# Performance work log

Hardware: AMD Instinct MI355X
Metric: run time of the kernel (lower is better)

Reference implementation:

```python
import jax, jax.numpy as jnp
import numpy as np

BSZ, L, D_Q, S_Q = 2, 2048, 512, 4
EPS = 1e-6


def quat_mul(a, b):
    ar, ai, aj, ak = a[..., 0], a[..., 1], a[..., 2], a[..., 3]
    br, bi, bj, bk = b[..., 0], b[..., 1], b[..., 2], b[..., 3]
    return jnp.stack((
        ar * br - ai * bi - aj * bj - ak * bk,
        ar * bi + ai * br + aj * bk - ak * bj,
        ar * bj - ai * bk + aj * br + ak * bi,
        ar * bk + ai * bj - aj * bi + ak * br,
    ), axis=-1)


def quat_inv(q):
    r, i, j, k = q[..., 0], q[..., 1], q[..., 2], q[..., 3]
    s = 1.0 / (r * r + i * i + j * j + k * k + EPS)
    return jnp.stack((r * s, -i * s, -j * s, -k * s), axis=-1)


def setup_inputs() -> dict:
    key = jax.random.key(0)
    ks = jax.random.split(key, 8)
    u = jax.random.normal(ks[0], (BSZ, L, D_Q, 4), dtype=jnp.float32)
    dt = jax.random.uniform(ks[1], (BSZ, L, D_Q), dtype=jnp.float32)
    B_in = jax.random.normal(ks[2], (BSZ, L, S_Q, 4), dtype=jnp.float32)
    C_in = jax.random.normal(ks[3], (BSZ, L, S_Q, 4), dtype=jnp.float32)
    # A_log init: log(arange(1, S_q+1)) repeated over D_q rows
    A_log = jnp.tile(jnp.log(jnp.arange(1, S_Q + 1, dtype=jnp.float32)), (D_Q, 1))
    A_i = jax.random.normal(ks[4], (D_Q, S_Q), dtype=jnp.float32) * 0.01
    A_j = jax.random.normal(ks[5], (D_Q, S_Q), dtype=jnp.float32) * 0.01
    A_k = jax.random.normal(ks[6], (D_Q, S_Q), dtype=jnp.float32) * 0.01
    return {"u": u, "dt": dt, "B_in": B_in, "C_in": C_in,
            "A_log": A_log, "A_i": A_i, "A_j": A_j, "A_k": A_k}


def reference(u, dt, B_in, C_in, A_log, A_i, A_j, A_k):
    # A quaternion: real part -exp(A_log), imaginary parts A_i/j/k  [D_q, S_q, 4]
    A_quat = jnp.stack([-jnp.exp(A_log), A_i, A_j, A_k], axis=-1)
    dt_b = dt[..., None, None]                      # [B, L, D_q, 1, 1]
    z = dt_b * A_quat                               # [B, L, D_q, S_q, 4]
    one = jnp.zeros_like(z).at[..., 0].set(1.0)     # quaternion identity
    num = one + 0.5 * z
    den = one - 0.5 * z
    den_inv = quat_inv(den)
    q = quat_mul(den_inv, num)                      # Cayley transition [B,L,D_q,S_q,4]
    dB = quat_mul(den_inv * dt_b, B_in[:, :, None])  # [B,L,D_q,S_q,4]
    Bu = quat_mul(dB, u[:, :, :, None])             # [B,L,D_q,S_q,4]

    def step(h, qb):
        qt, but = qb
        h = quat_mul(qt, h) + but
        return h, h

    h0 = jnp.zeros((u.shape[0], u.shape[2], A_quat.shape[1], 4), u.dtype)
    _, h_all = jax.lax.scan(step, h0, (jnp.swapaxes(q, 0, 1), jnp.swapaxes(Bu, 0, 1)))
    h_all = jnp.swapaxes(h_all, 0, 1)               # [B, L, D_q, S_q, 4]
    yh = quat_mul(C_in[:, :, None], h_all)
    return yh.sum(axis=3)                           # [B, L, D_q, 4]
```

## Files before the change

### kernel.cpp

```cpp
#include <hip/hip_runtime.h>

#define BSZ   2
#define LSEQ  2048
#define DQ    512
#define SQ    4
#define EPSQ  1e-6f

typedef float nfloat4 __attribute__((ext_vector_type(4)));
typedef float nfloat2 __attribute__((ext_vector_type(2)));

__device__ __forceinline__ nfloat2 mk2(float x, float y) { nfloat2 v; v.x = x; v.y = y; return v; }

struct PQuat { nfloat2 ri, jk; };

__device__ __forceinline__ PQuat pq_of(const float4 v) {
    PQuat p; p.ri = mk2(v.x, v.y); p.jk = mk2(v.z, v.w); return p;
}
__device__ __forceinline__ float4 f4_of(const PQuat p) {
    return make_float4(p.ri.x, p.ri.y, p.jk.x, p.jk.y);
}

__device__ __forceinline__ PQuat pqmul(const PQuat a, const PQuat b) {
    const float ar = a.ri.x, ai = a.ri.y, aj = a.jk.x, ak = a.jk.y;
    PQuat o;
    o.ri = ar*b.ri + ai*mk2(-b.ri.y,  b.ri.x)
         + aj*mk2(-b.jk.x,  b.jk.y) + ak*mk2(-b.jk.y, -b.jk.x);
    o.jk = ar*b.jk + ai*mk2(-b.jk.y,  b.jk.x)
         + aj*mk2( b.ri.x, -b.ri.y) + ak*mk2( b.ri.y,  b.ri.x);
    return o;
}

__device__ __forceinline__ PQuat pqmuladd(const PQuat a, const PQuat b, const PQuat c) {
    const float ar = a.ri.x, ai = a.ri.y, aj = a.jk.x, ak = a.jk.y;
    PQuat o;
    o.ri = c.ri + ar*b.ri + ai*mk2(-b.ri.y,  b.ri.x)
         + aj*mk2(-b.jk.x,  b.jk.y) + ak*mk2(-b.jk.y, -b.jk.x);
    o.jk = c.jk + ar*b.jk + ai*mk2(-b.jk.y,  b.jk.x)
         + aj*mk2( b.ri.x, -b.ri.y) + ak*mk2( b.ri.y,  b.ri.x);
    return o;
}

struct HA { float r, i; nfloat2 jk; float p2, n2r; };

__device__ __forceinline__ HA load_hA(const float* __restrict__ Alog,
                                      const float* __restrict__ Ai,
                                      const float* __restrict__ Aj,
                                      const float* __restrict__ Ak, int idx) {
    HA h;
    h.r  = -0.5f * __expf(Alog[idx]);
    h.i  =  0.5f * Ai[idx];
    h.jk = mk2(0.5f * Aj[idx], 0.5f * Ak[idx]);
    h.p2 = h.r*h.r + h.i*h.i + h.jk.x*h.jk.x + h.jk.y*h.jk.y;
    h.n2r = -2.0f * h.r;
    return h;
}

__device__ __forceinline__ void cayley_pk(const float a, const float aa, const HA& hA,
                                          const PQuat B, const PQuat U,
                                          PQuat& q, PQuat& Bu) {
    const float dd = __builtin_fmaf(aa, hA.p2, __builtin_fmaf(a, hA.n2r, 1.0f + EPSQ));
    const float sv = __builtin_amdgcn_rcpf(dd);
    const float nr = __builtin_fmaf(-aa, hA.p2, 1.0f);
    const float as = a * sv;
    const float s2a = as + as;
    q.ri = mk2(nr * sv, s2a * hA.i);
    q.jk = s2a * hA.jk;
    PQuat cd;
    cd.ri = mk2(__builtin_fmaf(-a, hA.r, 1.0f), a * hA.i);
    cd.jk = a * hA.jk;
    const PQuat cb = pqmul(cd, B);
    PQuat dB; dB.ri = as * cb.ri; dB.jk = as * cb.jk;
    Bu = pqmul(dB, U);
}

struct Quat { float r, i, j, k; };
__device__ __forceinline__ Quat qmul(const Quat a, const Quat b) {
    Quat o;
    o.r = a.r*b.r - a.i*b.i - a.j*b.j - a.k*b.k;
    o.i = a.r*b.i + a.i*b.r + a.j*b.k - a.k*b.j;
    o.j = a.r*b.j - a.i*b.k + a.j*b.r + a.k*b.i;
    o.k = a.r*b.k + a.i*b.j - a.j*b.i + a.k*b.r;
    return o;
}
__device__ __forceinline__ Quat qmuladd(const Quat a, const Quat b, const Quat c) {
    Quat o;
    o.r = c.r + a.r*b.r - a.i*b.i - a.j*b.j - a.k*b.k;
    o.i = c.i + a.r*b.i + a.i*b.r + a.j*b.k - a.k*b.j;
    o.j = c.j + a.r*b.j - a.i*b.k + a.j*b.r + a.k*b.i;
    o.k = c.k + a.r*b.k + a.i*b.j - a.j*b.i + a.k*b.r;
    return o;
}
__device__ __forceinline__ Quat q_of(const float4 v) { return Quat{v.x, v.y, v.z, v.w}; }
__device__ __forceinline__ float4 f4s_of(const Quat q) { return make_float4(q.r, q.i, q.j, q.k); }

typedef unsigned int u32_t;
__device__ __forceinline__ void gl_lds16(const void* g, void* l) {
    __builtin_amdgcn_global_load_lds(
        (const __attribute__((address_space(1))) u32_t*)g,
        (__attribute__((address_space(3))) u32_t*)l, 16, 0, 0);
}
__device__ __forceinline__ void gl_lds4(const void* g, void* l) {
    __builtin_amdgcn_global_load_lds(
        (const __attribute__((address_space(1))) u32_t*)g,
        (__attribute__((address_space(3))) u32_t*)l, 4, 0, 0);
}

template<int NCH>
__global__ __launch_bounds__(256, 6) void qssm_pass1(
    const float* __restrict__ u, const float* __restrict__ dt,
    const float* __restrict__ Bin,
    const float* __restrict__ Alog, const float* __restrict__ Ai,
    const float* __restrict__ Aj,   const float* __restrict__ Ak,
    float4* __restrict__ WQ, float4* __restrict__ WB)
{
    constexpr int CH = LSEQ / NCH;
    __shared__ float4 uL[CH][128];
    __shared__ float  dtL[CH][128];
    __shared__ float4 BL[CH][SQ];

    const int t    = threadIdx.x;
    const int lane = t & 63;
    const int wid  = t >> 6;
    const int dblk = blockIdx.x;
    const int c    = blockIdx.y;
    const int b    = blockIdx.z;
    const int t0   = c * CH;
    const int base = b*LSEQ + t0;

    const float4* ug  = (const float4*)u + (size_t)base*DQ + dblk*128;
    const float*  dtg = dt + (size_t)base*DQ + dblk*128;
    const float*  Bg  = Bin + (size_t)base*SQ*4;
#pragma unroll
    for (int jj = 0; jj < CH/4; ++jj) {
        const int j = wid*(CH/4) + jj;
#pragma unroll
        for (int k = 0; k < 2; ++k) {
            gl_lds16(ug  + (size_t)j*DQ + k*64 + lane, &uL[j][k*64]);
            gl_lds4 (dtg + (size_t)j*DQ + k*64 + lane, &dtL[j][k*64]);
        }
    }
    if (wid == 0) {
#pragma unroll
        for (int k = 0; k < 2; ++k)
            gl_lds4(Bg + k*64 + lane, ((float*)BL) + k*64);
    }

    const int dl = t & 127;
    const int sh = t >> 7;
    const int s0 = sh * 2;
    const int d  = dblk*128 + dl;

    HA hA0 = load_hA(Alog, Ai, Aj, Ak, d*SQ + s0);
    HA hA1 = load_hA(Alog, Ai, Aj, Ak, d*SQ + s0 + 1);

    __syncthreads();

    PQuat Q[2], Bc[2];
    {
        const float a  = dtL[0][dl];
        const float aa = a * a;
        const PQuat U  = pq_of(uL[0][dl]);
        PQuat q, Bu;
        cayley_pk(a, aa, hA0, pq_of(BL[0][s0]),     U, q, Bu);
        Q[0] = q; Bc[0] = Bu;
        cayley_pk(a, aa, hA1, pq_of(BL[0][s0 + 1]), U, q, Bu);
        Q[1] = q; Bc[1] = Bu;
    }
#pragma unroll
    for (int j = 1; j < CH; ++j) {
        const float a  = dtL[j][dl];
        const float aa = a * a;
        const PQuat U  = pq_of(uL[j][dl]);
        PQuat q, Bu;
        cayley_pk(a, aa, hA0, pq_of(BL[j][s0]),     U, q, Bu);
        Bc[0] = pqmuladd(q, Bc[0], Bu);
        Q[0]  = pqmul(q, Q[0]);
        cayley_pk(a, aa, hA1, pq_of(BL[j][s0 + 1]), U, q, Bu);
        Bc[1] = pqmuladd(q, Bc[1], Bu);
        Q[1]  = pqmul(q, Q[1]);
    }
#pragma unroll
    for (int ss = 0; ss < 2; ++ss) {
        const size_t idx = ((size_t)(b*SQ + s0 + ss)*NCH + c)*DQ + d;
        WQ[idx] = f4_of(Q[ss]);
        WB[idx] = f4_of(Bc[ss]);
    }
}

template<int NCH>
__global__ __launch_bounds__(512) void qssm_pass2(
    const float4* __restrict__ WQ, float4* __restrict__ WB)
{
    constexpr int GS = 8;
    constexpr int NG = NCH / GS;
    __shared__ float4 QL[NG][16];
    __shared__ float4 BL2[NG][16];
    __shared__ float4 HS[NG][16];

    const int t  = threadIdx.x;
    const int i  = t & 15;
    const int g  = t >> 4;
    const int bs = blockIdx.x >> 5;
    const int d  = (blockIdx.x & 31) * 16 + i;
    const size_t chbase = (size_t)bs * NCH * DQ + d;

    size_t idx = chbase + (size_t)(g * GS) * DQ;
    Quat Qa = q_of(WQ[idx]);
    Quat Ba = q_of(WB[idx]);
#pragma unroll
    for (int j = 1; j < GS; ++j) {
        idx += DQ;
        const Quat Qc = q_of(WQ[idx]);
        const Quat Bc = q_of(WB[idx]);
        Ba = qmuladd(Qc, Ba, Bc);
        Qa = qmul(Qc, Qa);
    }
    QL[g][i]  = f4s_of(Qa);
    BL2[g][i] = f4s_of(Ba);
    __syncthreads();

    if (t < 16) {
        Quat h{0.f, 0.f, 0.f, 0.f};
#pragma unroll
        for (int gg = 0; gg < NG; ++gg) {
            HS[gg][t] = f4s_of(h);
            h = qmuladd(q_of(QL[gg][t]), h, q_of(BL2[gg][t]));
        }
    }
    __syncthreads();

    Quat h = q_of(HS[g][i]);
    idx = chbase + (size_t)(g * GS) * DQ;
#pragma unroll
    for (int j = 0; j < GS; ++j) {
        const Quat Qc = q_of(WQ[idx]);
        const Quat Bc = q_of(WB[idx]);
        WB[idx] = f4s_of(h);
        h = qmuladd(Qc, h, Bc);
        idx += DQ;
    }
}

template<int NCH>
__global__ __launch_bounds__(256, 6) void qssm_pass3(
    const float* __restrict__ u, const float* __restrict__ dt,
    const float* __restrict__ Bin, const float* __restrict__ Cin,
    const float* __restrict__ Alog, const float* __restrict__ Ai,
    const float* __restrict__ Aj,   const float* __restrict__ Ak,
    const float4* __restrict__ WB, float* __restrict__ out)
{
    constexpr int CH = LSEQ / NCH;
    __shared__ float4 uL[CH][128];
    __shared__ float  dtL[CH][128];
    __shared__ float4 BL[CH][SQ];
    __shared__ float4 CL[CH][SQ];

    const int t    = threadIdx.x;
    const int lane = t & 63;
    const int wid  = t >> 6;
    const int dblk = blockIdx.x;
    const int c    = blockIdx.y;
    const int b    = blockIdx.z;
    const int t0   = c * CH;
    const int base = b*LSEQ + t0;

    const float4* ug  = (const float4*)u + (size_t)base*DQ + dblk*128;
    const float*  dtg = dt + (size_t)base*DQ + dblk*128;
    const float*  Bg  = Bin + (size_t)base*SQ*4;
    const float*  Cg  = Cin + (size_t)base*SQ*4;
#pragma unroll
    for (int jj = 0; jj < CH/4; ++jj) {
        const int j = wid*(CH/4) + jj;
#pragma unroll
        for (int k = 0; k < 2; ++k) {
            gl_lds16(ug  + (size_t)j*DQ + k*64 + lane, &uL[j][k*64]);
            gl_lds4 (dtg + (size_t)j*DQ + k*64 + lane, &dtL[j][k*64]);
        }
    }
    if (wid == 0) {
#pragma unroll
        for (int k = 0; k < 2; ++k)
            gl_lds4(Bg + k*64 + lane, ((float*)BL) + k*64);
    } else if (wid == 1) {
#pragma unroll
        for (int k = 0; k < 2; ++k)
            gl_lds4(Cg + k*64 + lane, ((float*)CL) + k*64);
    }

    const int dl = lane & 31;
    const int sh = lane >> 5;
    const int s0 = sh * 2;
    const int dloc = wid*32 + dl;
    const int d    = dblk*128 + dloc;

    HA hA0 = load_hA(Alog, Ai, Aj, Ak, d*SQ + s0);
    HA hA1 = load_hA(Alog, Ai, Aj, Ak, d*SQ + s0 + 1);
    PQuat h0 = pq_of(WB[((size_t)(b*SQ + s0    )*NCH + c)*DQ + d]);
    PQuat h1 = pq_of(WB[((size_t)(b*SQ + s0 + 1)*NCH + c)*DQ + d]);

    nfloat4* outp = (nfloat4*)out + (size_t)base*DQ + d;

    __syncthreads();

#pragma unroll
    for (int j = 0; j < CH; ++j) {
        const float a  = dtL[j][dloc];
        const float aa = a * a;
        const PQuat U  = pq_of(uL[j][dloc]);
        PQuat y; y.ri = mk2(0.f, 0.f); y.jk = mk2(0.f, 0.f);
        PQuat q, Bu;
        cayley_pk(a, aa, hA0, pq_of(BL[j][s0]),     U, q, Bu);
        h0 = pqmuladd(q, h0, Bu);
        y  = pqmuladd(pq_of(CL[j][s0]),     h0, y);
        cayley_pk(a, aa, hA1, pq_of(BL[j][s0 + 1]), U, q, Bu);
        h1 = pqmuladd(q, h1, Bu);
        y  = pqmuladd(pq_of(CL[j][s0 + 1]), h1, y);
        float yr = y.ri.x + __shfl_xor(y.ri.x, 32);
        float yi = y.ri.y + __shfl_xor(y.ri.y, 32);
        float yj = y.jk.x + __shfl_xor(y.jk.x, 32);
        float yk = y.jk.y + __shfl_xor(y.jk.y, 32);
        if (sh == 0) {
            const nfloat4 yv = {yr, yi, yj, yk};
            __builtin_nontemporal_store(yv, outp);
        }
        outp += DQ;
    }
}

template<int NCH>
static void launch_all(const float* u, const float* dt, const float* Bin,
                       const float* Cin, const float* Alog, const float* Ai,
                       const float* Aj, const float* Ak,
                       float* out, void* d_ws, hipStream_t stream) {
    const size_t elems = (size_t)BSZ * SQ * NCH * DQ;
    float4* WQ = (float4*)d_ws;
    float4* WB = WQ + elems;
    dim3 g1(DQ / 128, NCH, BSZ);
    qssm_pass1<NCH><<<g1, 256, 0, stream>>>(u, dt, Bin, Alog, Ai, Aj, Ak, WQ, WB);
    qssm_pass2<NCH><<<(BSZ*SQ*DQ)/16, 16*(NCH/8), 0, stream>>>(WQ, WB);
    dim3 g3(DQ / 128, NCH, BSZ);
    qssm_pass3<NCH><<<g3, 256, 0, stream>>>(u, dt, Bin, Cin, Alog, Ai, Aj, Ak, WB, out);
}

extern "C" void kernel_launch(void* const* d_in, const int* in_sizes, int n_in,
                              void* d_out, int out_size, void* d_ws, size_t ws_size,
                              hipStream_t stream) {
    const float* u    = (const float*)d_in[0];
    const float* dt   = (const float*)d_in[1];
    const float* Bin  = (const float*)d_in[2];
    const float* Cin  = (const float*)d_in[3];
    const float* Alog = (const float*)d_in[4];
    const float* Ai   = (const float*)d_in[5];
    const float* Aj   = (const float*)d_in[6];
    const float* Ak   = (const float*)d_in[7];
    float* out = (float*)d_out;

    auto ws_need = [](int nch) -> size_t {
        return 2ull * BSZ * SQ * (size_t)nch * DQ * sizeof(float4);
    };
    if (ws_size >= ws_need(256)) {
        launch_all<256>(u, dt, Bin, Cin, Alog, Ai, Aj, Ak, out, d_ws, stream);
    } else if (ws_size >= ws_need(128)) {
        launch_all<128>(u, dt, Bin, Cin, Alog, Ai, Aj, Ak, out, d_ws, stream);
    } else {
        launch_all<64>(u, dt, Bin, Cin, Alog, Ai, Aj, Ak, out, d_ws, stream);
    }
}
```

Baseline: 151.7 us.

## Fuse three-pass chunked scan into one cooperative kernel with grid syncs

```diff
diff --git a/kernel.cpp b/kernel.cpp
--- a/kernel.cpp
+++ b/kernel.cpp
@@ -1,4 +1,7 @@
 #include <hip/hip_runtime.h>
+#include <hip/hip_cooperative_groups.h>
+
+namespace cg = cooperative_groups;
 
 #define BSZ   2
 #define LSEQ  2048
@@ -105,6 +108,186 @@
         (__attribute__((address_space(3))) u32_t*)l, 4, 0, 0);
 }
 
+#define NCHF 256
+#define CHF  (LSEQ / NCHF)
+#define NTF  (BSZ * NCHF * (DQ/128))
+
+union SMemF {
+    struct { float4 uL[CHF][128]; float dtL[CHF][128];
+             float4 BL[CHF][SQ];   float4 CL[CHF][SQ]; } ac;
+    struct { float4 QL[32][16]; float4 BL2[32][16]; float4 HS[32][16]; } b;
+};
+
+__global__ __launch_bounds__(512, 4) void qssm_fused2(
+    const float* __restrict__ u, const float* __restrict__ dt,
+    const float* __restrict__ Bin, const float* __restrict__ Cin,
+    const float* __restrict__ Alog, const float* __restrict__ Ai,
+    const float* __restrict__ Aj,   const float* __restrict__ Ak,
+    float4* __restrict__ WQ, float4* __restrict__ WB, float* __restrict__ out)
+{
+    __shared__ SMemF sm;
+    cg::grid_group grid = cg::this_grid();
+    const int t    = threadIdx.x;
+    const int lane = t & 63;
+    const int wid  = t >> 6;
+
+    {
+        const int dl = t & 127;
+        const int sq = t >> 7;
+        for (int tid = blockIdx.x; tid < NTF; tid += (int)gridDim.x) {
+            const int dblk = tid & 3;
+            const int c    = (tid >> 2) & (NCHF - 1);
+            const int b    =  tid >> 10;
+            const int base = b*LSEQ + c*CHF;
+
+            __syncthreads();
+            const float4* ug  = (const float4*)u + (size_t)base*DQ + dblk*128;
+            const float*  dtg = dt + (size_t)base*DQ + dblk*128;
+            const float*  Bg  = Bin + (size_t)base*SQ*4;
+            {
+                const int j = wid;
+#pragma unroll
+                for (int k = 0; k < 2; ++k) {
+                    gl_lds16(ug  + (size_t)j*DQ + k*64 + lane, &sm.ac.uL[j][k*64]);
+                    gl_lds4 (dtg + (size_t)j*DQ + k*64 + lane, &sm.ac.dtL[j][k*64]);
+                }
+            }
+            if (wid == 0) {
+#pragma unroll
+                for (int k = 0; k < (CHF*SQ*4)/64; ++k)
+                    gl_lds4(Bg + k*64 + lane, ((float*)sm.ac.BL) + k*64);
+            }
+            const int d = dblk*128 + dl;
+            const HA hA = load_hA(Alog, Ai, Aj, Ak, d*SQ + sq);
+            __syncthreads();
+
+            PQuat Q, Bc;
+            {
+                const float a = sm.ac.dtL[0][dl];
+                cayley_pk(a, a*a, hA, pq_of(sm.ac.BL[0][sq]), pq_of(sm.ac.uL[0][dl]), Q, Bc);
+            }
+#pragma unroll
+            for (int j = 1; j < CHF; ++j) {
+                const float a = sm.ac.dtL[j][dl];
+                PQuat q, Bu;
+                cayley_pk(a, a*a, hA, pq_of(sm.ac.BL[j][sq]), pq_of(sm.ac.uL[j][dl]), q, Bu);
+                Bc = pqmuladd(q, Bc, Bu);
+                Q  = pqmul(q, Q);
+            }
+            const size_t idx = ((size_t)(b*SQ + sq)*NCHF + c)*DQ + d;
+            WQ[idx] = f4_of(Q);
+            WB[idx] = f4_of(Bc);
+        }
+    }
+    grid.sync();
+
+    if (blockIdx.x < 256) {
+        constexpr int GS = 8;
+        constexpr int NG = NCHF / GS;
+        const int i  = t & 15;
+        const int g  = t >> 4;
+        const int bs = blockIdx.x >> 5;
+        const int d  = (blockIdx.x & 31) * 16 + i;
+        const size_t chbase = (size_t)bs * NCHF * DQ + d;
+
+        size_t idx = chbase + (size_t)(g * GS) * DQ;
+        Quat Qa = q_of(WQ[idx]);
+        Quat Ba = q_of(WB[idx]);
+#pragma unroll
+        for (int j = 1; j < GS; ++j) {
+            idx += DQ;
+            const Quat Qc = q_of(WQ[idx]);
+            const Quat Bc = q_of(WB[idx]);
+            Ba = qmuladd(Qc, Ba, Bc);
+            Qa = qmul(Qc, Qa);
+        }
+        sm.b.QL[g][i]  = f4s_of(Qa);
+        sm.b.BL2[g][i] = f4s_of(Ba);
+        __syncthreads();
+
+        if (t < 16) {
+            Quat h{0.f, 0.f, 0.f, 0.f};
+#pragma unroll
+            for (int gg = 0; gg < NG; ++gg) {
+                sm.b.HS[gg][t] = f4s_of(h);
+                h = qmuladd(q_of(sm.b.QL[gg][t]), h, q_of(sm.b.BL2[gg][t]));
+            }
+        }
+        __syncthreads();
+
+        Quat h = q_of(sm.b.HS[g][i]);
+        idx = chbase + (size_t)(g * GS) * DQ;
+#pragma unroll
+        for (int j = 0; j < GS; ++j) {
+            const Quat Qc = q_of(WQ[idx]);
+            const Quat Bc = q_of(WB[idx]);
+            WB[idx] = f4s_of(h);
+            h = qmuladd(Qc, h, Bc);
+            idx += DQ;
+        }
+    }
+    grid.sync();
+
+    {
+        const int dl   = lane & 15;
+        const int sq   = lane >> 4;
+        const int dloc = wid*16 + dl;
+        for (int tid = blockIdx.x; tid < NTF; tid += (int)gridDim.x) {
+            const int dblk = tid & 3;
+            const int c    = (tid >> 2) & (NCHF - 1);
+            const int b    =  tid >> 10;
+            const int base = b*LSEQ + c*CHF;
+
+            __syncthreads();
+            const float4* ug  = (const float4*)u + (size_t)base*DQ + dblk*128;
+            const float*  dtg = dt + (size_t)base*DQ + dblk*128;
+            const float*  Bg  = Bin + (size_t)base*SQ*4;
+            const float*  Cg  = Cin + (size_t)base*SQ*4;
+            {
+                const int j = wid;
+#pragma unroll
+                for (int k = 0; k < 2; ++k) {
+                    gl_lds16(ug  + (size_t)j*DQ + k*64 + lane, &sm.ac.uL[j][k*64]);
+                    gl_lds4 (dtg + (size_t)j*DQ + k*64 + lane, &sm.ac.dtL[j][k*64]);
+                }
+            }
+            if (wid == 0) {
+#pragma unroll
+                for (int k = 0; k < (CHF*SQ*4)/64; ++k)
+                    gl_lds4(Bg + k*64 + lane, ((float*)sm.ac.BL) + k*64);
+            } else if (wid == 1) {
+#pragma unroll
+                for (int k = 0; k < (CHF*SQ*4)/64; ++k)
+                    gl_lds4(Cg + k*64 + lane, ((float*)sm.ac.CL) + k*64);
+            }
+            const int d = dblk*128 + dloc;
+            const HA hA = load_hA(Alog, Ai, Aj, Ak, d*SQ + sq);
+            PQuat h = pq_of(WB[((size_t)(b*SQ + sq)*NCHF + c)*DQ + d]);
+            nfloat4* outp = (nfloat4*)out + (size_t)base*DQ + d;
+            __syncthreads();
+
+#pragma unroll
+            for (int j = 0; j < CHF; ++j) {
+                const float a = sm.ac.dtL[j][dloc];
+                PQuat q, Bu;
+                cayley_pk(a, a*a, hA, pq_of(sm.ac.BL[j][sq]), pq_of(sm.ac.uL[j][dloc]), q, Bu);
+                h = pqmuladd(q, h, Bu);
+                const PQuat y = pqmul(pq_of(sm.ac.CL[j][sq]), h);
+                float yr = y.ri.x, yi = y.ri.y, yj = y.jk.x, yk = y.jk.y;
+                yr += __shfl_xor(yr, 16); yi += __shfl_xor(yi, 16);
+                yj += __shfl_xor(yj, 16); yk += __shfl_xor(yk, 16);
+                yr += __shfl_xor(yr, 32); yi += __shfl_xor(yi, 32);
+                yj += __shfl_xor(yj, 32); yk += __shfl_xor(yk, 32);
+                if (sq == 0) {
+                    const nfloat4 yv = {yr, yi, yj, yk};
+                    __builtin_nontemporal_store(yv, outp);
+                }
+                outp += DQ;
+            }
+        }
+    }
+}
+
 template<int NCH>
 __global__ __launch_bounds__(256, 6) void qssm_pass1(
     const float* __restrict__ u, const float* __restrict__ dt,
@@ -124,8 +307,7 @@
     const int dblk = blockIdx.x;
     const int c    = blockIdx.y;
     const int b    = blockIdx.z;
-    const int t0   = c * CH;
-    const int base = b*LSEQ + t0;
+    const int base = b*LSEQ + c*CH;
 
     const float4* ug  = (const float4*)u + (size_t)base*DQ + dblk*128;
     const float*  dtg = dt + (size_t)base*DQ + dblk*128;
@@ -261,8 +443,7 @@
     const int dblk = blockIdx.x;
     const int c    = blockIdx.y;
     const int b    = blockIdx.z;
-    const int t0   = c * CH;
-    const int base = b*LSEQ + t0;
+    const int base = b*LSEQ + c*CH;
 
     const float4* ug  = (const float4*)u + (size_t)base*DQ + dblk*128;
     const float*  dtg = dt + (size_t)base*DQ + dblk*128;
@@ -287,9 +468,9 @@
             gl_lds4(Cg + k*64 + lane, ((float*)CL) + k*64);
     }
 
-    const int dl = lane & 31;
-    const int sh = lane >> 5;
-    const int s0 = sh * 2;
+    const int dl   = lane & 31;
+    const int sh   = lane >> 5;
+    const int s0   = sh * 2;
     const int dloc = wid*32 + dl;
     const int d    = dblk*128 + dloc;
 
@@ -355,6 +536,20 @@
     const float* Ak   = (const float*)d_in[7];
     float* out = (float*)d_out;
 
+    const size_t elemsF = (size_t)BSZ * SQ * NCHF * DQ;
+    if (ws_size >= 2 * elemsF * sizeof(float4)) {
+        float4* WQ = (float4*)d_ws;
+        float4* WB = WQ + elemsF;
+        void* kargs[] = {(void*)&u, (void*)&dt, (void*)&Bin, (void*)&Cin,
+                         (void*)&Alog, (void*)&Ai, (void*)&Aj, (void*)&Ak,
+                         (void*)&WQ, (void*)&WB, (void*)&out};
+        hipError_t e = hipLaunchCooperativeKernel(
+            reinterpret_cast<void*>(qssm_fused2),
+            dim3(512), dim3(512), kargs, 0, stream);
+        if (e == hipSuccess) return;
+        (void)hipGetLastError();
+    }
+
     auto ws_need = [](int nch) -> size_t {
         return 2ull * BSZ * SQ * (size_t)nch * DQ * sizeof(float4);
     };
```

Result: slower. 297.2 us (+95.9%).
